# Kernel tuning notes

Hardware: AMD Instinct MI355X
Metric: run time of the kernel (lower is better)

## Reference

```python
import jax, jax.numpy as jnp
import numpy as np

INPUT_DIM = 3
NUM_LEVELS = 16
LEVEL_DIM = 2
PER_LEVEL_SCALE = 2.0
BASE_RES = 16
LOG2_HASH = 19
ALIGN_CORNERS = False
STD = 1e-4
B = 250000
_PRIMES = (1, 2654435761, 805459861)  # fast_hash primes for D=3 (prime[0]=1)


def _compute_offsets():
    # exactly mirrors GridEncoder.__init__ offset computation
    offsets, offset = [], 0
    max_params = 2 ** LOG2_HASH
    for i in range(NUM_LEVELS):
        res = int(np.ceil(BASE_RES * PER_LEVEL_SCALE ** i))
        if not ALIGN_CORNERS:
            res += 1
        p = min(max_params, res ** INPUT_DIM)
        p = int(np.ceil(p / 8) * 8)
        offsets.append(offset)
        offset += p
    offsets.append(offset)
    return np.array(offsets, dtype=np.int32)


def setup_inputs() -> dict:
    key = jax.random.key(0)
    k1, k2 = jax.random.split(key)
    offsets = _compute_offsets()
    inputs = jax.random.uniform(k1, (B, INPUT_DIM), dtype=jnp.float32)
    embeddings = jax.random.uniform(k2, (int(offsets[-1]), LEVEL_DIM),
                                    dtype=jnp.float32, minval=-STD, maxval=STD)
    return {"inputs": inputs, "embeddings": embeddings, "offsets": jnp.asarray(offsets)}


def _encode(inputs, embeddings, offsets):
    Bn, D = inputs.shape
    L = offsets.shape[0] - 1
    C = embeddings.shape[1]
    S = float(np.log2(PER_LEVEL_SCALE))
    H = float(BASE_RES)

    levels = jnp.arange(L, dtype=jnp.float32)
    scales = jnp.exp2(levels * S) * H - 1.0                      # [L]
    res_f = jnp.ceil(scales) + 1.0                                # [L] kernel resolution
    res = res_f.astype(jnp.int32)
    hsize = (offsets[1:] - offsets[:-1]).astype(jnp.int32)        # [L] per-level table size
    use_hash = (res_f ** 3) > hsize.astype(jnp.float32)           # [L] dense grid fits?

    off = 0.0 if ALIGN_CORNERS else 0.5
    pos = inputs[None, :, :] * scales[:, None, None] + off        # [L,B,D]
    pg_f = jnp.floor(pos)
    frac = pos - pg_f                                             # [L,B,D]
    pg = pg_f.astype(jnp.int32)

    corners = jnp.array([[(c >> d) & 1 for d in range(D)]
                         for c in range(2 ** D)], dtype=jnp.int32)  # [8,D]
    cg = pg[:, :, None, :] + corners[None, None, :, :]            # [L,B,8,D]

    # dense (non-hashed) index: c0 + c1*R + c2*R^2; clamp R to 1 on hashed levels
    safe_res = jnp.where(use_hash, jnp.int32(1), res)
    stride = jnp.stack([jnp.ones_like(safe_res), safe_res, safe_res * safe_res], -1)  # [L,3]
    dense = (cg * stride[:, None, None, :]).sum(-1) % hsize[:, None, None]            # [L,B,8]

    # fast_hash (uint32 wraparound xor-of-products)
    cgu = cg.astype(jnp.uint32)
    primes = jnp.array(_PRIMES, dtype=jnp.uint32)
    h = (cgu[..., 0] * primes[0]) ^ (cgu[..., 1] * primes[1]) ^ (cgu[..., 2] * primes[2])
    hidx = (h % hsize.astype(jnp.uint32)[:, None, None]).astype(jnp.int32)

    idx = jnp.where(use_hash[:, None, None], hidx, dense) + offsets[:-1][:, None, None]  # [L,B,8]

    # trilinear weights
    cb = corners.astype(bool)[None, None, :, :]                   # [1,1,8,D]
    w = jnp.where(cb, frac[:, :, None, :], 1.0 - frac[:, :, None, :]).prod(-1)  # [L,B,8]

    vals = embeddings[idx]                                        # [L,B,8,C]
    out = jnp.einsum('lbk,lbkc->lbc', w, vals)                    # [L,B,C]
    return out.transpose(1, 0, 2).reshape(Bn, L * C)              # [B, L*C]


def reference(inputs, embeddings, offsets):
    return _encode(inputs, embeddings, offsets)
```

## Files before the change

kernel.cpp:

```cpp
#include <hip/hip_runtime.h>


constexpr int NLEV = 16;
constexpr int BLK  = 256;

template<bool TO_WS, bool PINNED>
__global__ __launch_bounds__(BLK) void grid_gather(
    const float* __restrict__ inputs,
    const float2* __restrict__ emb,
    const int* __restrict__ offsets,
    float2* __restrict__ dst,
    int B, int chunks)
{
    const float SCALES[NLEV] = {
        15.f, 31.f, 63.f, 127.f, 255.f, 511.f, 1023.f, 2047.f,
        4095.f, 8191.f, 16383.f, 32767.f, 65535.f,
        131071.0625f,
        262143.f,
        524286.75f
    };

    int l, chunk;
    if (PINNED) {
        int xcd = blockIdx.x & 7;
        int j   = blockIdx.x >> 3;
        if (j < chunks) { l = xcd;      chunk = j; }
        else            { l = 15 - xcd; chunk = j - chunks; }
    } else {
        l = blockIdx.x / chunks;
        chunk = blockIdx.x - l * chunks;
    }
    int b = chunk * BLK + threadIdx.x;
    if (b >= B) return;

    float x = inputs[(size_t)b * 3 + 0];
    float y = inputs[(size_t)b * 3 + 1];
    float z = inputs[(size_t)b * 3 + 2];

    int off0  = offsets[l];
    int hsize = offsets[l + 1] - off0;
    int res   = 16 << l;
    float scale = SCALES[l];
    long long r3 = (long long)res * res * res;
    bool use_hash = r3 > (long long)hsize;
    uint32_t uh   = (uint32_t)hsize;
    bool     pow2 = (uh & (uh - 1u)) == 0u;

    float px = __fadd_rn(__fmul_rn(x, scale), 0.5f);
    float py = __fadd_rn(__fmul_rn(y, scale), 0.5f);
    float pz = __fadd_rn(__fmul_rn(z, scale), 0.5f);
    float gx = floorf(px), gy = floorf(py), gz = floorf(pz);
    float fx = __fsub_rn(px, gx), fy = __fsub_rn(py, gy), fz = __fsub_rn(pz, gz);
    int pgx = (int)gx, pgy = (int)gy, pgz = (int)gz;
    float omx = __fsub_rn(1.0f, fx), omy = __fsub_rn(1.0f, fy), omz = __fsub_rn(1.0f, fz);

    float r0 = 0.0f, r1 = 0.0f;
    const float2* tab = emb + (size_t)off0;

    if (use_hash && pow2) {
        const uint32_t mask = uh - 1u;
        #pragma unroll
        for (int k2 = 0; k2 < 4; ++k2) {
            const int by = k2 & 1, bz = (k2 >> 1) & 1;
            uint32_t m = ((uint32_t)(pgy + by) * 2654435761u)
                       ^ ((uint32_t)(pgz + bz) * 805459861u);
            uint32_t i0 = ((uint32_t)pgx ^ m) & mask;
            uint32_t i1 = ((uint32_t)(pgx + 1) ^ m) & mask;
            float4 q0 = *(const float4*)(tab + (i0 & ~1u));
            float4 q1 = *(const float4*)(tab + (i1 & ~1u));
            float2 v0 = (i0 & 1u) ? make_float2(q0.z, q0.w) : make_float2(q0.x, q0.y);
            float2 v1 = (i1 & 1u) ? make_float2(q1.z, q1.w) : make_float2(q1.x, q1.y);
            float wy = by ? fy : omy;
            float wz = bz ? fz : omz;
            float w0 = __fmul_rn(__fmul_rn(omx, wy), wz);
            float w1 = __fmul_rn(__fmul_rn(fx,  wy), wz);
            r0 = __fadd_rn(r0, __fmul_rn(w0, v0.x));
            r1 = __fadd_rn(r1, __fmul_rn(w0, v0.y));
            r0 = __fadd_rn(r0, __fmul_rn(w1, v1.x));
            r1 = __fadd_rn(r1, __fmul_rn(w1, v1.y));
        }
    } else {
        #pragma unroll
        for (int k2 = 0; k2 < 4; ++k2) {
            const int by = k2 & 1, bz = (k2 >> 1) & 1;
            int di0 = pgx + (pgy + by) * res + (pgz + bz) * res * res;
            uint32_t i0 = (uint32_t)(di0 % hsize);
            uint32_t i1 = (uint32_t)((di0 + 1) % hsize);
            float4 q0 = *(const float4*)(tab + (i0 & ~1u));
            float4 q1 = *(const float4*)(tab + (i1 & ~1u));
            float2 v0 = (i0 & 1u) ? make_float2(q0.z, q0.w) : make_float2(q0.x, q0.y);
            float2 v1 = (i1 & 1u) ? make_float2(q1.z, q1.w) : make_float2(q1.x, q1.y);
            float wy = by ? fy : omy;
            float wz = bz ? fz : omz;
            float w0 = __fmul_rn(__fmul_rn(omx, wy), wz);
            float w1 = __fmul_rn(__fmul_rn(fx,  wy), wz);
            r0 = __fadd_rn(r0, __fmul_rn(w0, v0.x));
            r1 = __fadd_rn(r1, __fmul_rn(w0, v0.y));
            r0 = __fadd_rn(r0, __fmul_rn(w1, v1.x));
            r1 = __fadd_rn(r1, __fmul_rn(w1, v1.y));
        }
    }

    if (TO_WS)
        dst[(size_t)l * B + b] = make_float2(r0, r1);
    else
        dst[(size_t)b * NLEV + l] = make_float2(r0, r1);
}

__global__ __launch_bounds__(256) void transpose_lds(
    const float4* __restrict__ ws4,
    float4* __restrict__ out4,
    int B)
{
    __shared__ float2 lds[64][17];
    int halfB = B >> 1;
    int b0 = blockIdx.x * 64;
    int t = threadIdx.x;

    #pragma unroll
    for (int rep = 0; rep < 2; ++rep) {
        int idx = t + rep * 256;
        int l = idx >> 5, p = idx & 31;
        int gp = (b0 >> 1) + p;
        if (gp < halfB) {
            float4 q = ws4[(size_t)l * halfB + gp];
            lds[2 * p][l]     = make_float2(q.x, q.y);
            lds[2 * p + 1][l] = make_float2(q.z, q.w);
        }
    }
    __syncthreads();

    #pragma unroll
    for (int rep = 0; rep < 2; ++rep) {
        int idx = t + rep * 256;
        int pt = idx >> 3, c = idx & 7;
        int gb = b0 + pt;
        if (gb < B) {
            float2 a  = lds[pt][2 * c];
            float2 b2 = lds[pt][2 * c + 1];
            out4[(size_t)gb * 8 + c] = make_float4(a.x, a.y, b2.x, b2.y);
        }
    }
}

__global__ __launch_bounds__(256) void transpose_out1(
    const float2* __restrict__ ws,
    float2* __restrict__ out,
    int B)
{
    int b = blockIdx.x * 256 + threadIdx.x;
    if (b >= B) return;
    float2 v[NLEV];
    #pragma unroll
    for (int l = 0; l < NLEV; ++l)
        v[l] = ws[(size_t)l * B + b];
    float4* o = (float4*)(out + (size_t)b * NLEV);
    #pragma unroll
    for (int i = 0; i < 8; ++i)
        o[i] = make_float4(v[2*i].x, v[2*i].y, v[2*i+1].x, v[2*i+1].y);
}

extern "C" void kernel_launch(void* const* d_in, const int* in_sizes, int n_in,
                              void* d_out, int out_size, void* d_ws, size_t ws_size,
                              hipStream_t stream) {
    const float*  inputs  = (const float*)d_in[0];
    const float2* emb     = (const float2*)d_in[1];
    const int*    offsets = (const int*)d_in[2];
    float2*       out     = (float2*)d_out;
    int B = in_sizes[0] / 3;
    int chunks = (B + BLK - 1) / BLK;
    int grid = NLEV * chunks;

    bool use_ws = ws_size >= (size_t)B * NLEV * sizeof(float2);
    if (use_ws) {
        float2* ws = (float2*)d_ws;
        hipLaunchKernelGGL((grid_gather<true, true>), dim3(grid), dim3(BLK), 0, stream,
                           inputs, emb, offsets, ws, B, chunks);
        if ((B & 1) == 0) {
            hipLaunchKernelGGL(transpose_lds, dim3((B + 63) / 64), dim3(256), 0, stream,
                               (const float4*)ws, (float4*)out, B);
        } else {
            hipLaunchKernelGGL(transpose_out1, dim3((B + 255) / 256), dim3(256), 0, stream,
                               ws, out, B);
        }
    } else {
        hipLaunchKernelGGL((grid_gather<false, false>), dim3(grid), dim3(BLK), 0, stream,
                           inputs, emb, offsets, out, B, chunks);
    }
}
```

Before: 125.2 us.

## Weight-balance level/chunk work across XCDs and skip duplicate float4 loads

```diff
diff --git a/kernel.cpp b/kernel.cpp
--- a/kernel.cpp
+++ b/kernel.cpp
@@ -4,7 +4,25 @@
 constexpr int NLEV = 16;
 constexpr int BLK  = 256;
 
-template<bool TO_WS, bool PINNED>
+__host__ __device__ inline int sched_boundary(int x, int K) {
+    const int Wt[16] = {1,8,10,10,10,10,10,10,10,10,10,10,10,10,10,10};
+    long long WT = 0;
+    for (int l = 0; l < 16; ++l) WT += (long long)K * Wt[l];
+    long long target = (long long)x * WT;
+    long long pref = 0;
+    for (int l = 0; l < 16; ++l) {
+        long long lvlW = (long long)K * Wt[l];
+        if (8 * (pref + lvlW) >= target) {
+            long long need = target - 8 * pref;
+            long long t = need <= 0 ? 0 : (need + 8LL * Wt[l] - 1) / (8LL * Wt[l]);
+            return (int)((long long)l * K + t);
+        }
+        pref += lvlW;
+    }
+    return 16 * K;
+}
+
+template<bool TO_WS, bool BALANCED>
 __global__ __launch_bounds__(BLK) void grid_gather(
     const float* __restrict__ inputs,
     const float2* __restrict__ emb,
@@ -21,11 +39,15 @@
     };
 
     int l, chunk;
-    if (PINNED) {
+    if (BALANCED) {
         int xcd = blockIdx.x & 7;
         int j   = blockIdx.x >> 3;
-        if (j < chunks) { l = xcd;      chunk = j; }
-        else            { l = 15 - xcd; chunk = j - chunks; }
+        int s0 = sched_boundary(xcd, chunks);
+        int s1 = sched_boundary(xcd + 1, chunks);
+        int c = s0 + j;
+        if (c >= s1) return;
+        l = c / chunks;
+        chunk = c - l * chunks;
     } else {
         l = blockIdx.x / chunks;
         chunk = blockIdx.x - l * chunks;
@@ -66,8 +88,11 @@
                        ^ ((uint32_t)(pgz + bz) * 805459861u);
             uint32_t i0 = ((uint32_t)pgx ^ m) & mask;
             uint32_t i1 = ((uint32_t)(pgx + 1) ^ m) & mask;
-            float4 q0 = *(const float4*)(tab + (i0 & ~1u));
-            float4 q1 = *(const float4*)(tab + (i1 & ~1u));
+            uint32_t la0 = i0 & ~1u, la1 = i1 & ~1u;
+            float4 q0 = *(const float4*)(tab + la0);
+            float4 q1;
+            if (la1 != la0) q1 = *(const float4*)(tab + la1);
+            else            q1 = q0;
             float2 v0 = (i0 & 1u) ? make_float2(q0.z, q0.w) : make_float2(q0.x, q0.y);
             float2 v1 = (i1 & 1u) ? make_float2(q1.z, q1.w) : make_float2(q1.x, q1.y);
             float wy = by ? fy : omy;
@@ -86,8 +111,11 @@
             int di0 = pgx + (pgy + by) * res + (pgz + bz) * res * res;
             uint32_t i0 = (uint32_t)(di0 % hsize);
             uint32_t i1 = (uint32_t)((di0 + 1) % hsize);
-            float4 q0 = *(const float4*)(tab + (i0 & ~1u));
-            float4 q1 = *(const float4*)(tab + (i1 & ~1u));
+            uint32_t la0 = i0 & ~1u, la1 = i1 & ~1u;
+            float4 q0 = *(const float4*)(tab + la0);
+            float4 q1;
+            if (la1 != la0) q1 = *(const float4*)(tab + la1);
+            else            q1 = q0;
             float2 v0 = (i0 & 1u) ? make_float2(q0.z, q0.w) : make_float2(q0.x, q0.y);
             float2 v1 = (i1 & 1u) ? make_float2(q1.z, q1.w) : make_float2(q1.x, q1.y);
             float wy = by ? fy : omy;
@@ -169,10 +197,17 @@
     float2*       out     = (float2*)d_out;
     int B = in_sizes[0] / 3;
     int chunks = (B + BLK - 1) / BLK;
-    int grid = NLEV * chunks;
 
     bool use_ws = ws_size >= (size_t)B * NLEV * sizeof(float2);
     if (use_ws) {
+        int maxC = 0;
+        int prev = sched_boundary(0, chunks);
+        for (int x = 1; x <= 8; ++x) {
+            int s = sched_boundary(x, chunks);
+            if (s - prev > maxC) maxC = s - prev;
+            prev = s;
+        }
+        int grid = 8 * maxC;
         float2* ws = (float2*)d_ws;
         hipLaunchKernelGGL((grid_gather<true, true>), dim3(grid), dim3(BLK), 0, stream,
                            inputs, emb, offsets, ws, B, chunks);
@@ -184,7 +219,7 @@
                                ws, out, B);
         }
     } else {
-        hipLaunchKernelGGL((grid_gather<false, false>), dim3(grid), dim3(BLK), 0, stream,
+        hipLaunchKernelGGL((grid_gather<false, false>), dim3(NLEV * chunks), dim3(BLK), 0, stream,
                            inputs, emb, offsets, out, B, chunks);
     }
 }
```

Result: slower. 155.0 us (+23.8%).
